# Kernel tuning notes

Measured on AMD Instinct MI355X. Metric: run time of the kernel, lower is better.

## Reference

```python
import jax, jax.numpy as jnp
import numpy as np

BATCH = 1048576
D_IN = 4        # d_in=3 spatial dims + 1 time dim
HID = 64
N_HID_STACK = 4  # hidden residual blocks after the first hidden layer
D_OUT = 3
BN_EPS = 1e-5


def _bn(x, gamma, beta):
    # BatchNorm1d in training mode: biased batch statistics over the batch axis
    mu = jnp.mean(x, axis=0)
    var = jnp.var(x, axis=0)
    return gamma * (x - mu) * jax.lax.rsqrt(var + BN_EPS) + beta


def setup_inputs() -> dict:
    key = jax.random.key(0)
    ks = jax.random.split(key, 8)
    s_in = 1.0 / np.sqrt(D_IN)
    s_h = 1.0 / np.sqrt(HID)
    return {
        "x": jax.random.normal(ks[0], (BATCH, D_IN), dtype=jnp.float32),
        "bn0_gamma": jnp.ones((D_IN,), jnp.float32),
        "bn0_beta": jnp.zeros((D_IN,), jnp.float32),
        "W0": jax.random.normal(ks[1], (D_IN, HID), jnp.float32) * s_in,
        "b0": jnp.zeros((HID,), jnp.float32),
        "gamma0": jnp.ones((HID,), jnp.float32),
        "beta0": jnp.zeros((HID,), jnp.float32),
        "W_hid": jax.random.normal(ks[2], (N_HID_STACK, HID, HID), jnp.float32) * s_h,
        "b_hid": jnp.zeros((N_HID_STACK, HID), jnp.float32),
        "gamma_hid": jnp.ones((N_HID_STACK, HID), jnp.float32),
        "beta_hid": jnp.zeros((N_HID_STACK, HID), jnp.float32),
        "Wout": jax.random.normal(ks[3], (HID, D_OUT), jnp.float32) * s_h,
        "bout": jnp.zeros((D_OUT,), jnp.float32),
    }


def reference(x, bn0_gamma, bn0_beta, W0, b0, gamma0, beta0,
              W_hid, b_hid, gamma_hid, beta_hid, Wout, bout):
    # Net.forward (u-network, single patch, batch_normalization=True, tanh):
    #   x = bn0(x)
    #   y = bn(act(Linear0(x)))                 (first hidden layer, no skip)
    #   y = bn_i(act(Linear_i(y))) + y          (residual hidden layers)
    #   y = Linear_out(y)
    h = _bn(x, bn0_gamma, bn0_beta)
    y = _bn(jnp.tanh(h @ W0 + b0), gamma0, beta0)

    def step(y, layer):
        W, b, g, be = layer
        return _bn(jnp.tanh(y @ W + b), g, be) + y, None

    y, _ = jax.lax.scan(step, y, (W_hid, b_hid, gamma_hid, beta_hid))
    return y @ Wout + bout
```

## Files before the change

### kernel.cpp

```cpp
#include <hip/hip_runtime.h>
#include <stdint.h>


#define NROWS 1048576
#define EPS 1e-5f
#define INV_B 9.5367431640625e-07f
#define LOG2E2 2.885390081777927f
#define BIGGRID 16384

typedef __attribute__((ext_vector_type(8))) short bfrag;
typedef __attribute__((ext_vector_type(4))) float facc;
typedef __attribute__((ext_vector_type(4))) float f4v;

__device__ __forceinline__ float bf2f(short s) {
  union { unsigned u; float f; } v;
  v.u = ((unsigned)(unsigned short)s) << 16;
  return v.f;
}
__device__ __forceinline__ short f2bf(float f) {
  union { float f; unsigned u; } v;
  v.f = f;
  unsigned r = v.u + 0x7FFFu + ((v.u >> 16) & 1u);
  return (short)(r >> 16);
}
__device__ __forceinline__ float tanh_fast(float x) {
  float e = __builtin_amdgcn_exp2f(x * LOG2E2);
  return 1.f - 2.f * __builtin_amdgcn_rcpf(e + 1.f);
}

template <int W>
__global__ __launch_bounds__(256) void k_reduce(const float* __restrict__ P,
                                                float* __restrict__ S,
                                                int rows_per_blk) {
  __shared__ float red[256];
  const int tid = threadIdx.x;
  const int col = tid % W;
  const int grp = tid / W;
  const int G = 256 / W;
  size_t r0 = (size_t)blockIdx.x * rows_per_blk;
  float s = 0.f;
  for (int r = grp; r < rows_per_blk; r += G) s += P[(r0 + r) * W + col];
  red[tid] = s;
  __syncthreads();
  if (tid < W) {
    float t = 0.f;
#pragma unroll 4
    for (int g = 0; g < G; ++g) t += red[g * W + tid];
    atomicAdd(&S[tid], t);
  }
}


__global__ __launch_bounds__(256) void k_stats_x(const float* __restrict__ x,
                                                 float* __restrict__ P) {
  __shared__ float red[4][8];
  const int tid = threadIdx.x;
  const int wave = tid >> 6;
  size_t base = (size_t)blockIdx.x * 1024 + tid;
  float s[4] = {0.f, 0.f, 0.f, 0.f}, q[4] = {0.f, 0.f, 0.f, 0.f};
#pragma unroll
  for (int it = 0; it < 4; ++it) {
    f4v v = *(const f4v*)(x + (base + (size_t)it * 256) * 4);
#pragma unroll
    for (int k = 0; k < 4; ++k) { s[k] += v[k]; q[k] = fmaf(v[k], v[k], q[k]); }
  }
#pragma unroll
  for (int off = 32; off > 0; off >>= 1) {
#pragma unroll
    for (int k = 0; k < 4; ++k) {
      s[k] += __shfl_xor(s[k], off);
      q[k] += __shfl_xor(q[k], off);
    }
  }
  if ((tid & 63) == 0) {
#pragma unroll
    for (int k = 0; k < 4; ++k) { red[wave][k] = s[k]; red[wave][4 + k] = q[k]; }
  }
  __syncthreads();
  if (tid < 8)
    P[blockIdx.x * 8 + tid] =
        red[0][tid] + red[1][tid] + red[2][tid] + red[3][tid];
}

__global__ __launch_bounds__(256) void k_stats_z1(
    const float* __restrict__ x, const float* __restrict__ bn0g,
    const float* __restrict__ bn0b, const float* __restrict__ W0,
    const float* __restrict__ b0, const float* __restrict__ sx,
    float* __restrict__ P) {
  __shared__ float red[2][4][64];
  const int tid = threadIdx.x;
  const int lane = tid & 63;
  const int wave = tid >> 6;
  int gw = blockIdx.x * 4 + wave;
  float sc[4], sh[4];
#pragma unroll
  for (int k = 0; k < 4; ++k) {
    float mean = sx[k] * INV_B;
    float var = fmaf(-mean, mean, sx[4 + k] * INV_B);
    float rs = rsqrtf(var + EPS);
    sc[k] = bn0g[k] * rs;
    sh[k] = fmaf(-sc[k], mean, bn0b[k]);
  }
  float w2[4];
  float b2 = b0[lane];
#pragma unroll
  for (int k = 0; k < 4; ++k) {
    float w = W0[k * 64 + lane];
    w2[k] = sc[k] * w;
    b2 = fmaf(sh[k], w, b2);
  }
  float s = 0.f, q = 0.f;
  size_t r0 = (size_t)gw * 256;
  for (int r = 0; r < 256; ++r) {
    f4v xv = *(const f4v*)(x + (r0 + r) * 4);
    float acc = b2;
#pragma unroll
    for (int k = 0; k < 4; ++k) acc = fmaf(xv[k], w2[k], acc);
    float z = tanh_fast(acc);
    s += z;
    q = fmaf(z, z, q);
  }
  red[0][wave][lane] = s;
  red[1][wave][lane] = q;
  __syncthreads();
  if (tid < 128) {
    int which = tid >> 6, c = tid & 63;
    P[blockIdx.x * 128 + tid] = red[which][0][c] + red[which][1][c] +
                                red[which][2][c] + red[which][3][c];
  }
}

__global__ __launch_bounds__(256) void k_prep(const float* __restrict__ Wh,
                                              short* __restrict__ WT) {
  int idx = blockIdx.x * 256 + threadIdx.x;
  int l = idx >> 12, rem = idx & 4095, k = rem >> 6, c = rem & 63;
  WT[l * 4096 + c * 64 + k] = f2bf(Wh[l * 4096 + k * 64 + c]);
}


__global__ __launch_bounds__(128) void k_first(
    const float* __restrict__ x, const float* __restrict__ bn0g,
    const float* __restrict__ bn0b, const float* __restrict__ W0,
    const float* __restrict__ b0, const float* __restrict__ gamma0,
    const float* __restrict__ beta0, const float* __restrict__ sx,
    const float* __restrict__ s1, const short* __restrict__ WTb,
    const float* __restrict__ bb, float* __restrict__ P,
    short* __restrict__ Y) {
  __shared__ __align__(16) float lds_x[64 * 4];
  __shared__ __align__(16) short lds_y[64 * 72];
  __shared__ float lds_st[128];

  const int tid = threadIdx.x;
  const int lane = tid & 63;
  const int wave = tid >> 6;
  const int l15 = lane & 15;
  const int q = lane >> 4;
  const int wr = wave * 32;
  const size_t r0 = (size_t)blockIdx.x * 64;

  f4v xp;
  if (lane < 32) xp = *(const f4v*)(x + (r0 + wr + lane) * 4);

  lds_st[tid] = 0.f;
  float sc0[4], sh0[4];
#pragma unroll
  for (int k = 0; k < 4; ++k) {
    float mean = sx[k] * INV_B;
    float var = fmaf(-mean, mean, sx[4 + k] * INV_B);
    float rs = rsqrtf(var + EPS);
    sc0[k] = bn0g[k] * rs;
    sh0[k] = fmaf(-sc0[k], mean, bn0b[k]);
  }
  float w2[4];
  float b2 = b0[lane];
#pragma unroll
  for (int k = 0; k < 4; ++k) {
    float w = W0[k * 64 + lane];
    w2[k] = sc0[k] * w;
    b2 = fmaf(sh0[k], w, b2);
  }
  float mean1 = s1[lane] * INV_B;
  float var1 = fmaf(-mean1, mean1, s1[64 + lane] * INV_B);
  float A1c = gamma0[lane] * rsqrtf(var1 + EPS);
  float B1c = fmaf(-A1c, mean1, beta0[lane]);
  if (lane < 32) *(f4v*)&lds_x[(wr + lane) * 4] = xp;
  __syncthreads();

  for (int e = 0; e < 32; ++e) {
    int row = wr + e;
    f4v xv = *(const f4v*)&lds_x[row * 4];
    float acc = b2;
#pragma unroll
    for (int k = 0; k < 4; ++k) acc = fmaf(xv[k], w2[k], acc);
    float z = tanh_fast(acc);
    lds_y[row * 72 + lane] = f2bf(fmaf(A1c, z, B1c));
  }

  bfrag af[2][2];
#pragma unroll
  for (int mt = 0; mt < 2; ++mt)
#pragma unroll
    for (int kt = 0; kt < 2; ++kt) {
      af[mt][kt] =
          *(const bfrag*)&lds_y[(wr + mt * 16 + l15) * 72 + kt * 32 + q * 8];
      *(bfrag*)(Y + (r0 + wr + mt * 16 + l15) * 64 + kt * 32 + q * 8) =
          af[mt][kt];
    }
  float bbv[4];
  bfrag bwb[4][2];
#pragma unroll
  for (int nt = 0; nt < 4; ++nt) {
    bbv[nt] = bb[nt * 16 + l15];
#pragma unroll
    for (int kt = 0; kt < 2; ++kt)
      bwb[nt][kt] =
          *(const bfrag*)(WTb + (nt * 16 + l15) * 64 + kt * 32 + q * 8);
  }
  facc acc2[2][4];
#pragma unroll
  for (int mt = 0; mt < 2; ++mt)
#pragma unroll
    for (int nt = 0; nt < 4; ++nt) {
      acc2[mt][nt][0] = bbv[nt]; acc2[mt][nt][1] = bbv[nt];
      acc2[mt][nt][2] = bbv[nt]; acc2[mt][nt][3] = bbv[nt];
    }
#pragma unroll
  for (int mt = 0; mt < 2; ++mt)
#pragma unroll
    for (int nt = 0; nt < 4; ++nt)
#pragma unroll
      for (int kt = 0; kt < 2; ++kt)
        acc2[mt][nt] = __builtin_amdgcn_mfma_f32_16x16x32_bf16(
            af[mt][kt], bwb[nt][kt], acc2[mt][nt], 0, 0, 0);
  float sAcc[4], qAcc[4];
#pragma unroll
  for (int nt = 0; nt < 4; ++nt) {
    sAcc[nt] = 0.f;
    qAcc[nt] = 0.f;
#pragma unroll
    for (int mt = 0; mt < 2; ++mt)
#pragma unroll
      for (int i = 0; i < 4; ++i) {
        float z = tanh_fast(acc2[mt][nt][i]);
        sAcc[nt] += z;
        qAcc[nt] = fmaf(z, z, qAcc[nt]);
      }
    float s = sAcc[nt], ss = qAcc[nt];
    s += __shfl_xor(s, 16); s += __shfl_xor(s, 32);
    ss += __shfl_xor(ss, 16); ss += __shfl_xor(ss, 32);
    if (q == 0) {
      atomicAdd(&lds_st[nt * 16 + l15], s);
      atomicAdd(&lds_st[64 + nt * 16 + l15], ss);
    }
  }
  __syncthreads();
  P[(size_t)blockIdx.x * 128 + tid] = lds_st[tid];
}

__global__ __launch_bounds__(128) void k_mid(
    short* __restrict__ Y, const short* __restrict__ WTa,
    const float* __restrict__ ba, const float* __restrict__ ga,
    const float* __restrict__ bea, const float* __restrict__ sa,
    const short* __restrict__ WTb, const float* __restrict__ bb,
    float* __restrict__ P) {
  __shared__ __align__(16) short lds_y[64 * 72];
  __shared__ float lds_st[128];

  const int tid = threadIdx.x;
  const int lane = tid & 63;
  const int wave = tid >> 6;
  const int l15 = lane & 15;
  const int q = lane >> 4;
  const int wr = wave * 32;
  const size_t r0 = (size_t)blockIdx.x * 64;
  const int srow = lane >> 3;
  const int sc8 = (lane & 7) * 8;

  bfrag ld[4];
  {
    const size_t g = (r0 + wr + srow) * 64 + sc8;
#pragma unroll
    for (int it = 0; it < 4; ++it)
      ld[it] = *(const bfrag*)(Y + g + (size_t)it * 8 * 64);
  }

  lds_st[tid] = 0.f;
  float Av[4], Bv[4], bav[4];
#pragma unroll
  for (int nt = 0; nt < 4; ++nt) {
    int c = nt * 16 + l15;
    float mean = sa[c] * INV_B;
    float var = fmaf(-mean, mean, sa[64 + c] * INV_B);
    float A = ga[c] * rsqrtf(var + EPS);
    Av[nt] = A;
    Bv[nt] = fmaf(-A, mean, bea[c]);
    bav[nt] = ba[c];
  }
  bfrag bwa[4][2];
#pragma unroll
  for (int nt = 0; nt < 4; ++nt)
#pragma unroll
    for (int kt = 0; kt < 2; ++kt)
      bwa[nt][kt] =
          *(const bfrag*)(WTa + (nt * 16 + l15) * 64 + kt * 32 + q * 8);

#pragma unroll
  for (int it = 0; it < 4; ++it)
    *(bfrag*)&lds_y[(wr + it * 8 + srow) * 72 + sc8] = ld[it];
  __syncthreads();

  bfrag af[2][2];
#pragma unroll
  for (int mt = 0; mt < 2; ++mt)
#pragma unroll
    for (int kt = 0; kt < 2; ++kt)
      af[mt][kt] =
          *(const bfrag*)&lds_y[(wr + mt * 16 + l15) * 72 + kt * 32 + q * 8];
  facc acc[2][4];
#pragma unroll
  for (int mt = 0; mt < 2; ++mt)
#pragma unroll
    for (int nt = 0; nt < 4; ++nt) {
      acc[mt][nt][0] = bav[nt]; acc[mt][nt][1] = bav[nt];
      acc[mt][nt][2] = bav[nt]; acc[mt][nt][3] = bav[nt];
    }
#pragma unroll
  for (int mt = 0; mt < 2; ++mt)
#pragma unroll
    for (int nt = 0; nt < 4; ++nt)
#pragma unroll
      for (int kt = 0; kt < 2; ++kt)
        acc[mt][nt] = __builtin_amdgcn_mfma_f32_16x16x32_bf16(
            af[mt][kt], bwa[nt][kt], acc[mt][nt], 0, 0, 0);

#pragma unroll
  for (int mt = 0; mt < 2; ++mt)
#pragma unroll
    for (int nt = 0; nt < 4; ++nt) {
      int c = nt * 16 + l15;
      float A = Av[nt], Bc = Bv[nt];
#pragma unroll
      for (int i = 0; i < 4; ++i) {
        int rl = wr + mt * 16 + q * 4 + i;
        float z = tanh_fast(acc[mt][nt][i]);
        float yo = bf2f(lds_y[rl * 72 + c]);
        lds_y[rl * 72 + c] = f2bf(fmaf(A, z, Bc) + yo);
      }
    }

#pragma unroll
  for (int mt = 0; mt < 2; ++mt)
#pragma unroll
    for (int kt = 0; kt < 2; ++kt) {
      af[mt][kt] =
          *(const bfrag*)&lds_y[(wr + mt * 16 + l15) * 72 + kt * 32 + q * 8];
      *(bfrag*)(Y + (r0 + wr + mt * 16 + l15) * 64 + kt * 32 + q * 8) =
          af[mt][kt];
    }
  float bbv[4];
  bfrag bwb[4][2];
#pragma unroll
  for (int nt = 0; nt < 4; ++nt) {
    bbv[nt] = bb[nt * 16 + l15];
#pragma unroll
    for (int kt = 0; kt < 2; ++kt)
      bwb[nt][kt] =
          *(const bfrag*)(WTb + (nt * 16 + l15) * 64 + kt * 32 + q * 8);
  }
#pragma unroll
  for (int mt = 0; mt < 2; ++mt)
#pragma unroll
    for (int nt = 0; nt < 4; ++nt) {
      acc[mt][nt][0] = bbv[nt]; acc[mt][nt][1] = bbv[nt];
      acc[mt][nt][2] = bbv[nt]; acc[mt][nt][3] = bbv[nt];
    }
#pragma unroll
  for (int mt = 0; mt < 2; ++mt)
#pragma unroll
    for (int nt = 0; nt < 4; ++nt)
#pragma unroll
      for (int kt = 0; kt < 2; ++kt)
        acc[mt][nt] = __builtin_amdgcn_mfma_f32_16x16x32_bf16(
            af[mt][kt], bwb[nt][kt], acc[mt][nt], 0, 0, 0);
#pragma unroll
  for (int nt = 0; nt < 4; ++nt) {
    float s = 0.f, ss = 0.f;
#pragma unroll
    for (int mt = 0; mt < 2; ++mt)
#pragma unroll
      for (int i = 0; i < 4; ++i) {
        float z = tanh_fast(acc[mt][nt][i]);
        s += z;
        ss = fmaf(z, z, ss);
      }
    s += __shfl_xor(s, 16); s += __shfl_xor(s, 32);
    ss += __shfl_xor(ss, 16); ss += __shfl_xor(ss, 32);
    if (q == 0) {
      atomicAdd(&lds_st[nt * 16 + l15], s);
      atomicAdd(&lds_st[64 + nt * 16 + l15], ss);
    }
  }
  __syncthreads();
  P[(size_t)blockIdx.x * 128 + tid] = lds_st[tid];
}

__global__ __launch_bounds__(128) void k_last(
    const short* __restrict__ Y, const short* __restrict__ WTa,
    const float* __restrict__ ba, const float* __restrict__ ga,
    const float* __restrict__ bea, const float* __restrict__ sa,
    const float* __restrict__ Wout, const float* __restrict__ bout,
    float* __restrict__ out) {
  __shared__ __align__(16) short lds_y[64 * 72];
  __shared__ float lds_wo[192];

  const int tid = threadIdx.x;
  const int lane = tid & 63;
  const int wave = tid >> 6;
  const int l15 = lane & 15;
  const int q = lane >> 4;
  const int wr = wave * 32;
  const size_t r0 = (size_t)blockIdx.x * 64;
  const int srow = lane >> 3;
  const int sc8 = (lane & 7) * 8;

  bfrag ld[4];
  {
    const size_t g = (r0 + wr + srow) * 64 + sc8;
#pragma unroll
    for (int it = 0; it < 4; ++it)
      ld[it] = *(const bfrag*)(Y + g + (size_t)it * 8 * 64);
  }

  for (int i = tid; i < 192; i += 128) lds_wo[i] = Wout[i];
  float Av[4], Bv[4], bav[4];
#pragma unroll
  for (int nt = 0; nt < 4; ++nt) {
    int c = nt * 16 + l15;
    float mean = sa[c] * INV_B;
    float var = fmaf(-mean, mean, sa[64 + c] * INV_B);
    float A = ga[c] * rsqrtf(var + EPS);
    Av[nt] = A;
    Bv[nt] = fmaf(-A, mean, bea[c]);
    bav[nt] = ba[c];
  }
  bfrag bwa[4][2];
#pragma unroll
  for (int nt = 0; nt < 4; ++nt)
#pragma unroll
    for (int kt = 0; kt < 2; ++kt)
      bwa[nt][kt] =
          *(const bfrag*)(WTa + (nt * 16 + l15) * 64 + kt * 32 + q * 8);
  float bo0 = bout[0], bo1 = bout[1], bo2 = bout[2];

#pragma unroll
  for (int it = 0; it < 4; ++it)
    *(bfrag*)&lds_y[(wr + it * 8 + srow) * 72 + sc8] = ld[it];
  __syncthreads();

  bfrag af[2][2];
#pragma unroll
  for (int mt = 0; mt < 2; ++mt)
#pragma unroll
    for (int kt = 0; kt < 2; ++kt)
      af[mt][kt] =
          *(const bfrag*)&lds_y[(wr + mt * 16 + l15) * 72 + kt * 32 + q * 8];
  facc acc[2][4];
#pragma unroll
  for (int mt = 0; mt < 2; ++mt)
#pragma unroll
    for (int nt = 0; nt < 4; ++nt) {
      acc[mt][nt][0] = bav[nt]; acc[mt][nt][1] = bav[nt];
      acc[mt][nt][2] = bav[nt]; acc[mt][nt][3] = bav[nt];
    }
#pragma unroll
  for (int mt = 0; mt < 2; ++mt)
#pragma unroll
    for (int nt = 0; nt < 4; ++nt)
#pragma unroll
      for (int kt = 0; kt < 2; ++kt)
        acc[mt][nt] = __builtin_amdgcn_mfma_f32_16x16x32_bf16(
            af[mt][kt], bwa[nt][kt], acc[mt][nt], 0, 0, 0);
#pragma unroll
  for (int mt = 0; mt < 2; ++mt)
#pragma unroll
    for (int nt = 0; nt < 4; ++nt) {
      int c = nt * 16 + l15;
      float A = Av[nt], Bc = Bv[nt];
#pragma unroll
      for (int i = 0; i < 4; ++i) {
        int rl = wr + mt * 16 + q * 4 + i;
        float z = tanh_fast(acc[mt][nt][i]);
        float yo = bf2f(lds_y[rl * 72 + c]);
        lds_y[rl * 72 + c] = f2bf(fmaf(A, z, Bc) + yo);
      }
    }

  {
    int row = wr + (lane >> 1);
    int cb = (lane & 1) * 32;
    float o0 = 0.f, o1 = 0.f, o2 = 0.f;
#pragma unroll
    for (int jc = 0; jc < 4; ++jc) {
      bfrag v = *(const bfrag*)&lds_y[row * 72 + cb + jc * 8];
#pragma unroll
      for (int j = 0; j < 8; ++j) {
        float f = bf2f(v[j]);
        int jj = cb + jc * 8 + j;
        o0 = fmaf(f, lds_wo[jj * 3 + 0], o0);
        o1 = fmaf(f, lds_wo[jj * 3 + 1], o1);
        o2 = fmaf(f, lds_wo[jj * 3 + 2], o2);
      }
    }
    o0 += __shfl_xor(o0, 1);
    o1 += __shfl_xor(o1, 1);
    o2 += __shfl_xor(o2, 1);
    if ((lane & 1) == 0) {
      size_t ro = (r0 + row) * 3;
      out[ro] = o0 + bo0;
      out[ro + 1] = o1 + bo1;
      out[ro + 2] = o2 + bo2;
    }
  }
}

extern "C" void kernel_launch(void* const* d_in, const int* in_sizes, int n_in,
                              void* d_out, int out_size, void* d_ws,
                              size_t ws_size, hipStream_t stream) {
  (void)in_sizes; (void)n_in; (void)out_size; (void)ws_size;
  const float* x = (const float*)d_in[0];
  const float* bn0g = (const float*)d_in[1];
  const float* bn0b = (const float*)d_in[2];
  const float* W0 = (const float*)d_in[3];
  const float* b0 = (const float*)d_in[4];
  const float* gamma0 = (const float*)d_in[5];
  const float* beta0 = (const float*)d_in[6];
  const float* Wh = (const float*)d_in[7];
  const float* bh = (const float*)d_in[8];
  const float* gh = (const float*)d_in[9];
  const float* beh = (const float*)d_in[10];
  const float* Wout = (const float*)d_in[11];
  const float* bout = (const float*)d_in[12];
  float* out = (float*)d_out;

  char* ws = (char*)d_ws;
  short* Y = (short*)ws;
  const size_t YB = (size_t)NROWS * 64 * 2;
  float* stats = (float*)(ws + YB);
  float* Sx = stats;
  float* S1 = stats + 8;
  float* S2 = stats + 136;
  float* S3 = stats + 264;
  float* S4 = stats + 392;
  float* S5 = stats + 520;
  short* WT = (short*)(ws + YB + 4096);
  float* P = (float*)(ws + YB + 4096 + 32768);

  hipMemsetAsync(stats, 0, 648 * sizeof(float), stream);
  k_prep<<<64, 256, 0, stream>>>(Wh, WT);
  k_stats_x<<<1024, 256, 0, stream>>>(x, P);
  k_reduce<8><<<8, 256, 0, stream>>>(P, Sx, 128);
  k_stats_z1<<<1024, 256, 0, stream>>>(x, bn0g, bn0b, W0, b0, Sx, P);
  k_reduce<128><<<8, 256, 0, stream>>>(P, S1, 128);
  k_first<<<BIGGRID, 128, 0, stream>>>(x, bn0g, bn0b, W0, b0, gamma0, beta0,
                                       Sx, S1, WT, bh, P, Y);
  k_reduce<128><<<128, 256, 0, stream>>>(P, S2, 128);
  k_mid<<<BIGGRID, 128, 0, stream>>>(Y, WT, bh, gh, beh, S2, WT + 4096,
                                     bh + 64, P);
  k_reduce<128><<<128, 256, 0, stream>>>(P, S3, 128);
  k_mid<<<BIGGRID, 128, 0, stream>>>(Y, WT + 4096, bh + 64, gh + 64, beh + 64,
                                     S3, WT + 2 * 4096, bh + 128, P);
  k_reduce<128><<<128, 256, 0, stream>>>(P, S4, 128);
  k_mid<<<BIGGRID, 128, 0, stream>>>(Y, WT + 2 * 4096, bh + 128, gh + 128,
                                     beh + 128, S4, WT + 3 * 4096, bh + 192, P);
  k_reduce<128><<<128, 256, 0, stream>>>(P, S5, 128);
  k_last<<<BIGGRID, 128, 0, stream>>>(Y, WT + 3 * 4096, bh + 192, gh + 192,
                                      beh + 192, S5, Wout, bout, out);
}
```

Measured before the change: 552.5 us.

## Load MFMA A-fragments directly from global and transpose residual via identity MFMA

In k_mid and k_last, the coalesced staging of Y through LDS is replaced by loading the MFMA A fragments straight from global memory. The residual values needed in the accumulator layout come from extra MFMAs against an identity matrix, so no LDS read-back is needed. This drops one barrier and the LDS round trip for the input tile. The LDS float atomics for the statistics reduction become per-wave slots summed at the end, at the cost of eight extra MFMAs per row tile and less coalesced global loads.

```diff
diff --git a/kernel.cpp b/kernel.cpp
--- a/kernel.cpp
+++ b/kernel.cpp
@@ -264,7 +264,7 @@
     const short* __restrict__ WTb, const float* __restrict__ bb,
     float* __restrict__ P) {
   __shared__ __align__(16) short lds_y[64 * 72];
-  __shared__ float lds_st[128];
+  __shared__ float red[2][128];
 
   const int tid = threadIdx.x;
   const int lane = tid & 63;
@@ -273,18 +273,15 @@
   const int q = lane >> 4;
   const int wr = wave * 32;
   const size_t r0 = (size_t)blockIdx.x * 64;
-  const int srow = lane >> 3;
-  const int sc8 = (lane & 7) * 8;
-
-  bfrag ld[4];
-  {
-    const size_t g = (r0 + wr + srow) * 64 + sc8;
-#pragma unroll
-    for (int it = 0; it < 4; ++it)
-      ld[it] = *(const bfrag*)(Y + g + (size_t)it * 8 * 64);
-  }
-
-  lds_st[tid] = 0.f;
+
+  bfrag af[2][2];
+#pragma unroll
+  for (int mt = 0; mt < 2; ++mt)
+#pragma unroll
+    for (int kt = 0; kt < 2; ++kt)
+      af[mt][kt] =
+          *(const bfrag*)(Y + (r0 + wr + mt * 16 + l15) * 64 + kt * 32 + q * 8);
+
   float Av[4], Bv[4], bav[4];
 #pragma unroll
   for (int nt = 0; nt < 4; ++nt) {
@@ -304,18 +301,14 @@
       bwa[nt][kt] =
           *(const bfrag*)(WTa + (nt * 16 + l15) * 64 + kt * 32 + q * 8);
 
-#pragma unroll
-  for (int it = 0; it < 4; ++it)
-    *(bfrag*)&lds_y[(wr + it * 8 + srow) * 72 + sc8] = ld[it];
-  __syncthreads();
-
-  bfrag af[2][2];
-#pragma unroll
-  for (int mt = 0; mt < 2; ++mt)
-#pragma unroll
-    for (int kt = 0; kt < 2; ++kt)
-      af[mt][kt] =
-          *(const bfrag*)&lds_y[(wr + mt * 16 + l15) * 72 + kt * 32 + q * 8];
+  const short one = (short)0x3F80;
+  bfrag id0, id1;
+#pragma unroll
+  for (int j = 0; j < 8; ++j) {
+    id0[j] = (q == (l15 >> 3) && (l15 & 7) == j) ? one : (short)0;
+    id1[j] = (q == 2 + (l15 >> 3) && (l15 & 7) == j) ? one : (short)0;
+  }
+
   facc acc[2][4];
 #pragma unroll
   for (int mt = 0; mt < 2; ++mt)
@@ -333,8 +326,14 @@
         acc[mt][nt] = __builtin_amdgcn_mfma_f32_16x16x32_bf16(
             af[mt][kt], bwa[nt][kt], acc[mt][nt], 0, 0, 0);
 
-#pragma unroll
-  for (int mt = 0; mt < 2; ++mt)
+  const facc zero4 = {0.f, 0.f, 0.f, 0.f};
+#pragma unroll
+  for (int mt = 0; mt < 2; ++mt) {
+    facc yv[4];
+#pragma unroll
+    for (int nt = 0; nt < 4; ++nt)
+      yv[nt] = __builtin_amdgcn_mfma_f32_16x16x32_bf16(
+          af[mt][nt >> 1], (nt & 1) ? id1 : id0, zero4, 0, 0, 0);
 #pragma unroll
     for (int nt = 0; nt < 4; ++nt) {
       int c = nt * 16 + l15;
@@ -343,11 +342,21 @@
       for (int i = 0; i < 4; ++i) {
         int rl = wr + mt * 16 + q * 4 + i;
         float z = tanh_fast(acc[mt][nt][i]);
-        float yo = bf2f(lds_y[rl * 72 + c]);
-        lds_y[rl * 72 + c] = f2bf(fmaf(A, z, Bc) + yo);
+        lds_y[rl * 72 + c] = f2bf(fmaf(A, z, Bc) + yv[nt][i]);
       }
     }
-
+  }
+
+  bfrag bwb[4][2];
+  float bbv[4];
+#pragma unroll
+  for (int nt = 0; nt < 4; ++nt) {
+    bbv[nt] = bb[nt * 16 + l15];
+#pragma unroll
+    for (int kt = 0; kt < 2; ++kt)
+      bwb[nt][kt] =
+          *(const bfrag*)(WTb + (nt * 16 + l15) * 64 + kt * 32 + q * 8);
+  }
 #pragma unroll
   for (int mt = 0; mt < 2; ++mt)
 #pragma unroll
@@ -357,22 +366,13 @@
       *(bfrag*)(Y + (r0 + wr + mt * 16 + l15) * 64 + kt * 32 + q * 8) =
           af[mt][kt];
     }
-  float bbv[4];
-  bfrag bwb[4][2];
-#pragma unroll
-  for (int nt = 0; nt < 4; ++nt) {
-    bbv[nt] = bb[nt * 16 + l15];
-#pragma unroll
-    for (int kt = 0; kt < 2; ++kt)
-      bwb[nt][kt] =
-          *(const bfrag*)(WTb + (nt * 16 + l15) * 64 + kt * 32 + q * 8);
-  }
+  facc acc2[2][4];
 #pragma unroll
   for (int mt = 0; mt < 2; ++mt)
 #pragma unroll
     for (int nt = 0; nt < 4; ++nt) {
-      acc[mt][nt][0] = bbv[nt]; acc[mt][nt][1] = bbv[nt];
-      acc[mt][nt][2] = bbv[nt]; acc[mt][nt][3] = bbv[nt];
+      acc2[mt][nt][0] = bbv[nt]; acc2[mt][nt][1] = bbv[nt];
+      acc2[mt][nt][2] = bbv[nt]; acc2[mt][nt][3] = bbv[nt];
     }
 #pragma unroll
   for (int mt = 0; mt < 2; ++mt)
@@ -380,8 +380,8 @@
     for (int nt = 0; nt < 4; ++nt)
 #pragma unroll
       for (int kt = 0; kt < 2; ++kt)
-        acc[mt][nt] = __builtin_amdgcn_mfma_f32_16x16x32_bf16(
-            af[mt][kt], bwb[nt][kt], acc[mt][nt], 0, 0, 0);
+        acc2[mt][nt] = __builtin_amdgcn_mfma_f32_16x16x32_bf16(
+            af[mt][kt], bwb[nt][kt], acc2[mt][nt], 0, 0, 0);
 #pragma unroll
   for (int nt = 0; nt < 4; ++nt) {
     float s = 0.f, ss = 0.f;
@@ -389,19 +389,19 @@
     for (int mt = 0; mt < 2; ++mt)
 #pragma unroll
       for (int i = 0; i < 4; ++i) {
-        float z = tanh_fast(acc[mt][nt][i]);
+        float z = tanh_fast(acc2[mt][nt][i]);
         s += z;
         ss = fmaf(z, z, ss);
       }
     s += __shfl_xor(s, 16); s += __shfl_xor(s, 32);
     ss += __shfl_xor(ss, 16); ss += __shfl_xor(ss, 32);
     if (q == 0) {
-      atomicAdd(&lds_st[nt * 16 + l15], s);
-      atomicAdd(&lds_st[64 + nt * 16 + l15], ss);
-    }
-  }
-  __syncthreads();
-  P[(size_t)blockIdx.x * 128 + tid] = lds_st[tid];
+      red[wave][nt * 16 + l15] = s;
+      red[wave][64 + nt * 16 + l15] = ss;
+    }
+  }
+  __syncthreads();
+  P[(size_t)blockIdx.x * 128 + tid] = red[0][tid] + red[1][tid];
 }
 
 __global__ __launch_bounds__(128) void k_last(
@@ -420,16 +420,14 @@
   const int q = lane >> 4;
   const int wr = wave * 32;
   const size_t r0 = (size_t)blockIdx.x * 64;
-  const int srow = lane >> 3;
-  const int sc8 = (lane & 7) * 8;
-
-  bfrag ld[4];
-  {
-    const size_t g = (r0 + wr + srow) * 64 + sc8;
-#pragma unroll
-    for (int it = 0; it < 4; ++it)
-      ld[it] = *(const bfrag*)(Y + g + (size_t)it * 8 * 64);
-  }
+
+  bfrag af[2][2];
+#pragma unroll
+  for (int mt = 0; mt < 2; ++mt)
+#pragma unroll
+    for (int kt = 0; kt < 2; ++kt)
+      af[mt][kt] =
+          *(const bfrag*)(Y + (r0 + wr + mt * 16 + l15) * 64 + kt * 32 + q * 8);
 
   for (int i = tid; i < 192; i += 128) lds_wo[i] = Wout[i];
   float Av[4], Bv[4], bav[4];
@@ -452,18 +450,15 @@
           *(const bfrag*)(WTa + (nt * 16 + l15) * 64 + kt * 32 + q * 8);
   float bo0 = bout[0], bo1 = bout[1], bo2 = bout[2];
 
-#pragma unroll
-  for (int it = 0; it < 4; ++it)
-    *(bfrag*)&lds_y[(wr + it * 8 + srow) * 72 + sc8] = ld[it];
-  __syncthreads();
-
-  bfrag af[2][2];
-#pragma unroll
-  for (int mt = 0; mt < 2; ++mt)
-#pragma unroll
-    for (int kt = 0; kt < 2; ++kt)
-      af[mt][kt] =
-          *(const bfrag*)&lds_y[(wr + mt * 16 + l15) * 72 + kt * 32 + q * 8];
+  const short one = (short)0x3F80;
+  bfrag id0, id1;
+#pragma unroll
+  for (int j = 0; j < 8; ++j) {
+    id0[j] = (q == (l15 >> 3) && (l15 & 7) == j) ? one : (short)0;
+    id1[j] = (q == 2 + (l15 >> 3) && (l15 & 7) == j) ? one : (short)0;
+  }
+  __syncthreads();
+
   facc acc[2][4];
 #pragma unroll
   for (int mt = 0; mt < 2; ++mt)
@@ -480,8 +475,15 @@
       for (int kt = 0; kt < 2; ++kt)
         acc[mt][nt] = __builtin_amdgcn_mfma_f32_16x16x32_bf16(
             af[mt][kt], bwa[nt][kt], acc[mt][nt], 0, 0, 0);
-#pragma unroll
-  for (int mt = 0; mt < 2; ++mt)
+
+  const facc zero4 = {0.f, 0.f, 0.f, 0.f};
+#pragma unroll
+  for (int mt = 0; mt < 2; ++mt) {
+    facc yv[4];
+#pragma unroll
+    for (int nt = 0; nt < 4; ++nt)
+      yv[nt] = __builtin_amdgcn_mfma_f32_16x16x32_bf16(
+          af[mt][nt >> 1], (nt & 1) ? id1 : id0, zero4, 0, 0, 0);
 #pragma unroll
     for (int nt = 0; nt < 4; ++nt) {
       int c = nt * 16 + l15;
@@ -490,10 +492,10 @@
       for (int i = 0; i < 4; ++i) {
         int rl = wr + mt * 16 + q * 4 + i;
         float z = tanh_fast(acc[mt][nt][i]);
-        float yo = bf2f(lds_y[rl * 72 + c]);
-        lds_y[rl * 72 + c] = f2bf(fmaf(A, z, Bc) + yo);
+        lds_y[rl * 72 + c] = f2bf(fmaf(A, z, Bc) + yv[nt][i]);
       }
     }
+  }
 
   {
     int row = wr + (lane >> 1);
```

Measured after the change: 585.7 us. 6.0% more time.

## Bucket BN partial stats with global atomics and load Y fragments directly

Applied to the files above, without the earlier changes.

Per-block BN partial sums are now atomically added into 256 global buckets per layer instead of written as 16384 separate rows, so the follow-up reduce kernels read far less data and launch fewer blocks. k_mid and k_last load their MFMA A-fragments straight from global memory in fragment layout, skipping the LDS round trip and one barrier in k_mid. k_mid also replaces LDS atomics for the stats with a plain per-wave array. The changes add global atomic contention, an extra memset, and non-deterministic float summation order.

```diff
diff --git a/kernel.cpp b/kernel.cpp
--- a/kernel.cpp
+++ b/kernel.cpp
@@ -7,6 +7,7 @@
 #define INV_B 9.5367431640625e-07f
 #define LOG2E2 2.885390081777927f
 #define BIGGRID 16384
+#define NBUCKET 256
 
 typedef __attribute__((ext_vector_type(8))) short bfrag;
 typedef __attribute__((ext_vector_type(4))) float facc;
@@ -144,7 +145,7 @@
     const float* __restrict__ b0, const float* __restrict__ gamma0,
     const float* __restrict__ beta0, const float* __restrict__ sx,
     const float* __restrict__ s1, const short* __restrict__ WTb,
-    const float* __restrict__ bb, float* __restrict__ P,
+    const float* __restrict__ bb, float* __restrict__ Pb,
     short* __restrict__ Y) {
   __shared__ __align__(16) float lds_x[64 * 4];
   __shared__ __align__(16) short lds_y[64 * 72];
@@ -254,7 +255,8 @@
     }
   }
   __syncthreads();
-  P[(size_t)blockIdx.x * 128 + tid] = lds_st[tid];
+  atomicAdd(&Pb[(size_t)(blockIdx.x & (NBUCKET - 1)) * 128 + tid],
+            lds_st[tid]);
 }
 
 __global__ __launch_bounds__(128) void k_mid(
@@ -262,9 +264,9 @@
     const float* __restrict__ ba, const float* __restrict__ ga,
     const float* __restrict__ bea, const float* __restrict__ sa,
     const short* __restrict__ WTb, const float* __restrict__ bb,
-    float* __restrict__ P) {
+    float* __restrict__ Pb) {
   __shared__ __align__(16) short lds_y[64 * 72];
-  __shared__ float lds_st[128];
+  __shared__ float red[2][128];
 
   const int tid = threadIdx.x;
   const int lane = tid & 63;
@@ -273,18 +275,15 @@
   const int q = lane >> 4;
   const int wr = wave * 32;
   const size_t r0 = (size_t)blockIdx.x * 64;
-  const int srow = lane >> 3;
-  const int sc8 = (lane & 7) * 8;
-
-  bfrag ld[4];
-  {
-    const size_t g = (r0 + wr + srow) * 64 + sc8;
-#pragma unroll
-    for (int it = 0; it < 4; ++it)
-      ld[it] = *(const bfrag*)(Y + g + (size_t)it * 8 * 64);
-  }
-
-  lds_st[tid] = 0.f;
+
+  bfrag af[2][2];
+#pragma unroll
+  for (int mt = 0; mt < 2; ++mt)
+#pragma unroll
+    for (int kt = 0; kt < 2; ++kt)
+      af[mt][kt] =
+          *(const bfrag*)(Y + (r0 + wr + mt * 16 + l15) * 64 + kt * 32 + q * 8);
+
   float Av[4], Bv[4], bav[4];
 #pragma unroll
   for (int nt = 0; nt < 4; ++nt) {
@@ -305,17 +304,12 @@
           *(const bfrag*)(WTa + (nt * 16 + l15) * 64 + kt * 32 + q * 8);
 
 #pragma unroll
-  for (int it = 0; it < 4; ++it)
-    *(bfrag*)&lds_y[(wr + it * 8 + srow) * 72 + sc8] = ld[it];
-  __syncthreads();
-
-  bfrag af[2][2];
-#pragma unroll
-  for (int mt = 0; mt < 2; ++mt)
-#pragma unroll
-    for (int kt = 0; kt < 2; ++kt)
-      af[mt][kt] =
-          *(const bfrag*)&lds_y[(wr + mt * 16 + l15) * 72 + kt * 32 + q * 8];
+  for (int mt = 0; mt < 2; ++mt)
+#pragma unroll
+    for (int kt = 0; kt < 2; ++kt)
+      *(bfrag*)&lds_y[(wr + mt * 16 + l15) * 72 + kt * 32 + q * 8] =
+          af[mt][kt];
+
   facc acc[2][4];
 #pragma unroll
   for (int mt = 0; mt < 2; ++mt)
@@ -396,12 +390,13 @@
     s += __shfl_xor(s, 16); s += __shfl_xor(s, 32);
     ss += __shfl_xor(ss, 16); ss += __shfl_xor(ss, 32);
     if (q == 0) {
-      atomicAdd(&lds_st[nt * 16 + l15], s);
-      atomicAdd(&lds_st[64 + nt * 16 + l15], ss);
-    }
-  }
-  __syncthreads();
-  P[(size_t)blockIdx.x * 128 + tid] = lds_st[tid];
+      red[wave][nt * 16 + l15] = s;
+      red[wave][64 + nt * 16 + l15] = ss;
+    }
+  }
+  __syncthreads();
+  atomicAdd(&Pb[(size_t)(blockIdx.x & (NBUCKET - 1)) * 128 + tid],
+            red[0][tid] + red[1][tid]);
 }
 
 __global__ __launch_bounds__(128) void k_last(
@@ -420,16 +415,14 @@
   const int q = lane >> 4;
   const int wr = wave * 32;
   const size_t r0 = (size_t)blockIdx.x * 64;
-  const int srow = lane >> 3;
-  const int sc8 = (lane & 7) * 8;
-
-  bfrag ld[4];
-  {
-    const size_t g = (r0 + wr + srow) * 64 + sc8;
-#pragma unroll
-    for (int it = 0; it < 4; ++it)
-      ld[it] = *(const bfrag*)(Y + g + (size_t)it * 8 * 64);
-  }
+
+  bfrag af[2][2];
+#pragma unroll
+  for (int mt = 0; mt < 2; ++mt)
+#pragma unroll
+    for (int kt = 0; kt < 2; ++kt)
+      af[mt][kt] =
+          *(const bfrag*)(Y + (r0 + wr + mt * 16 + l15) * 64 + kt * 32 + q * 8);
 
   for (int i = tid; i < 192; i += 128) lds_wo[i] = Wout[i];
   float Av[4], Bv[4], bav[4];
@@ -453,17 +446,13 @@
   float bo0 = bout[0], bo1 = bout[1], bo2 = bout[2];
 
 #pragma unroll
-  for (int it = 0; it < 4; ++it)
-    *(bfrag*)&lds_y[(wr + it * 8 + srow) * 72 + sc8] = ld[it];
-  __syncthreads();
-
-  bfrag af[2][2];
-#pragma unroll
-  for (int mt = 0; mt < 2; ++mt)
-#pragma unroll
-    for (int kt = 0; kt < 2; ++kt)
-      af[mt][kt] =
-          *(const bfrag*)&lds_y[(wr + mt * 16 + l15) * 72 + kt * 32 + q * 8];
+  for (int mt = 0; mt < 2; ++mt)
+#pragma unroll
+    for (int kt = 0; kt < 2; ++kt)
+      *(bfrag*)&lds_y[(wr + mt * 16 + l15) * 72 + kt * 32 + q * 8] =
+          af[mt][kt];
+  __syncthreads();
+
   facc acc[2][4];
 #pragma unroll
   for (int mt = 0; mt < 2; ++mt)
@@ -554,25 +543,32 @@
   float* S5 = stats + 520;
   short* WT = (short*)(ws + YB + 4096);
   float* P = (float*)(ws + YB + 4096 + 32768);
+  float* Pb = (float*)(ws + YB + 4096 + 32768 + (1 << 20));
+  float* Pb2 = Pb;
+  float* Pb3 = Pb + NBUCKET * 128;
+  float* Pb4 = Pb + 2 * NBUCKET * 128;
+  float* Pb5 = Pb + 3 * NBUCKET * 128;
 
   hipMemsetAsync(stats, 0, 648 * sizeof(float), stream);
+  hipMemsetAsync(Pb, 0, 4 * NBUCKET * 128 * sizeof(float), stream);
   k_prep<<<64, 256, 0, stream>>>(Wh, WT);
   k_stats_x<<<1024, 256, 0, stream>>>(x, P);
   k_reduce<8><<<8, 256, 0, stream>>>(P, Sx, 128);
   k_stats_z1<<<1024, 256, 0, stream>>>(x, bn0g, bn0b, W0, b0, Sx, P);
   k_reduce<128><<<8, 256, 0, stream>>>(P, S1, 128);
   k_first<<<BIGGRID, 128, 0, stream>>>(x, bn0g, bn0b, W0, b0, gamma0, beta0,
-                                       Sx, S1, WT, bh, P, Y);
-  k_reduce<128><<<128, 256, 0, stream>>>(P, S2, 128);
+                                       Sx, S1, WT, bh, Pb2, Y);
+  k_reduce<128><<<16, 256, 0, stream>>>(Pb2, S2, 16);
   k_mid<<<BIGGRID, 128, 0, stream>>>(Y, WT, bh, gh, beh, S2, WT + 4096,
-                                     bh + 64, P);
-  k_reduce<128><<<128, 256, 0, stream>>>(P, S3, 128);
+                                     bh + 64, Pb3);
+  k_reduce<128><<<16, 256, 0, stream>>>(Pb3, S3, 16);
   k_mid<<<BIGGRID, 128, 0, stream>>>(Y, WT + 4096, bh + 64, gh + 64, beh + 64,
-                                     S3, WT + 2 * 4096, bh + 128, P);
-  k_reduce<128><<<128, 256, 0, stream>>>(P, S4, 128);
+                                     S3, WT + 2 * 4096, bh + 128, Pb4);
+  k_reduce<128><<<16, 256, 0, stream>>>(Pb4, S4, 16);
   k_mid<<<BIGGRID, 128, 0, stream>>>(Y, WT + 2 * 4096, bh + 128, gh + 128,
-                                     beh + 128, S4, WT + 3 * 4096, bh + 192, P);
-  k_reduce<128><<<128, 256, 0, stream>>>(P, S5, 128);
+                                     beh + 128, S4, WT + 3 * 4096, bh + 192,
+                                     Pb5);
+  k_reduce<128><<<16, 256, 0, stream>>>(Pb5, S5, 16);
   k_last<<<BIGGRID, 128, 0, stream>>>(Y, WT + 3 * 4096, bh + 192, gh + 192,
                                       beh + 192, S5, Wout, bout, out);
 }
```

Result: faster. 534.3 us (-3.3%).
